# Kernel tuning notes

Measured on AMD Instinct MI355X. Metric: run time of the kernel, lower is better.

The kernel has to match this reference:

```python
import jax, jax.numpy as jnp
import numpy as np

NUM_NODES = 100000
NUM_EDGES = 1600000
FEAT = 128
HID = 128
NUM_GRAPHS = 512


def setup_inputs() -> dict:
    key = jax.random.key(0)
    ks = jax.random.split(key, 8)
    x = jax.random.normal(ks[0], (NUM_NODES, FEAT), dtype=jnp.float32)
    edge_index = jax.random.randint(ks[1], (2, NUM_EDGES), 0, NUM_NODES, dtype=jnp.int64)
    batch = jnp.sort(jax.random.randint(ks[2], (NUM_NODES,), 0, NUM_GRAPHS, dtype=jnp.int64))
    # Glorot-ish init for weights (scale named for clarity)
    s1 = 1.0 / np.sqrt(FEAT)
    s2 = 1.0 / np.sqrt(HID)
    W1 = jax.random.normal(ks[3], (FEAT, HID), dtype=jnp.float32) * s1
    b1 = jnp.zeros((HID,), dtype=jnp.float32)
    W2 = jax.random.normal(ks[4], (HID, HID), dtype=jnp.float32) * s2
    b2 = jnp.zeros((HID,), dtype=jnp.float32)
    Wout = jax.random.normal(ks[5], (HID, 1), dtype=jnp.float32) * s2
    bout = jnp.zeros((1,), dtype=jnp.float32)
    return {"x": x, "edge_index": edge_index, "batch": batch,
            "W1": W1, "b1": b1, "W2": W2, "b2": b2, "Wout": Wout, "bout": bout}


def reference(x, edge_index, batch, W1, b1, W2, b2, Wout, bout):
    N = x.shape[0]
    # PyG GCNConv: add self-loops, symmetric normalization D^-1/2 (A+I) D^-1/2
    loops = jnp.arange(N, dtype=edge_index.dtype)
    src = jnp.concatenate([edge_index[0], loops])  # [E+N]
    dst = jnp.concatenate([edge_index[1], loops])  # [E+N]
    ones = jnp.ones_like(dst, dtype=x.dtype)
    deg = jax.ops.segment_sum(ones, dst, num_segments=N)  # in-degree incl. self-loop
    dinv = jnp.where(deg > 0, jax.lax.rsqrt(deg), 0.0)
    coeff = (dinv[src] * dinv[dst])[:, None]  # [E+N, 1]

    def gcn(h, W, b):
        h = h @ W                                       # [N, H] dense GEMM
        msg = h[src] * coeff                            # gather + scale
        agg = jax.ops.segment_sum(msg, dst, num_segments=N)  # scatter-add
        return agg + b

    h = jax.nn.relu(gcn(x, W1, b1))
    h = jax.nn.relu(gcn(h, W2, b2))

    # global_mean_pool over batch ids
    G = NUM_GRAPHS
    sums = jax.ops.segment_sum(h, batch, num_segments=G)
    cnts = jax.ops.segment_sum(jnp.ones((N,), dtype=h.dtype), batch, num_segments=G)
    pooled = sums / jnp.maximum(cnts, 1.0)[:, None]

    return pooled @ Wout + bout  # [G, 1]
```

## Files before the change

kernel.cpp:

```cpp
#include <hip/hip_runtime.h>
#include <hip/hip_bf16.h>
#include <hip/hip_fp16.h>

#define FEAT 128
#define PSLOTS 64
#define BCAP 5120

typedef _Float16 h8 __attribute__((ext_vector_type(8)));
typedef float f4 __attribute__((ext_vector_type(4)));
typedef float fx2 __attribute__((ext_vector_type(2)));


__global__ __launch_bounds__(256) void k_wt(const float* __restrict__ W1,
                                            const float* __restrict__ W2,
                                            __half* __restrict__ Wt1,
                                            __half* __restrict__ Wt2) {
    int t = blockIdx.x * 256 + threadIdx.x;
    const float* W = (t < 8192) ? W1 : W2;
    __half* Wt     = (t < 8192) ? Wt1 : Wt2;
    int u = t & 8191;
    int n = u >> 6, k2 = (u & 63) * 2;
    float a = W[(size_t)k2 * 128 + n];
    float b = W[(size_t)(k2 + 1) * 128 + n];
    ((__half2*)Wt)[n * 64 + (k2 >> 1)] = __floats2half2_rn(a, b);
}


__device__ __forceinline__ void bin_body(const int* __restrict__ ei, int E, int chunk,
                                         int* __restrict__ cursor,
                                         unsigned* __restrict__ binned, int nb,
                                         int bid, int* smem) {
    int* hist = smem;
    int* base = smem + 512;
    int start = bid * chunk;
    int end = start + chunk; if (end > E) end = E;
    for (int i = threadIdx.x; i < nb; i += 256) hist[i] = 0;
    __syncthreads();
    for (int e = start + threadIdx.x; e < end; e += 256)
        atomicAdd(&hist[ei[E + e] >> 8], 1);
    __syncthreads();
    for (int i = threadIdx.x; i < nb; i += 256) {
        int h = hist[i];
        base[i] = h ? atomicAdd(&cursor[i], h) : 0;
    }
    __syncthreads();
    for (int e = start + threadIdx.x; e < end; e += 256) {
        int s = ei[e];
        int d = ei[E + e];
        int b = d >> 8;
        int pos = atomicAdd(&base[b], 1);
        if (pos < BCAP)
            binned[(size_t)b * BCAP + pos] = (unsigned)s | ((unsigned)(d & 255) << 17);
    }
}


__device__ __forceinline__ void loadA(const __half* p, int quad, h8* a) {
#pragma unroll
    for (int ks = 0; ks < 4; ++ks)
        a[ks] = *(const h8*)(p + ks * 32 + quad * 8);
}
__device__ __forceinline__ void loadA(const float* p, int quad, h8* a) {
#pragma unroll
    for (int ks = 0; ks < 4; ++ks) {
        const float* q = p + ks * 32 + quad * 8;
        float4 f0 = *(const float4*)q;
        float4 f1 = *(const float4*)(q + 4);
        h8 v;
        v[0] = (_Float16)f0.x; v[1] = (_Float16)f0.y;
        v[2] = (_Float16)f0.z; v[3] = (_Float16)f0.w;
        v[4] = (_Float16)f1.x; v[5] = (_Float16)f1.y;
        v[6] = (_Float16)f1.z; v[7] = (_Float16)f1.w;
        a[ks] = v;
    }
}

template <typename TIN>
__device__ __forceinline__ void gemm_body(const TIN* __restrict__ X,
                                          const __half* __restrict__ Wt,
                                          unsigned char* __restrict__ Y, int N,
                                          int bid, _Float16* Bs) {
    {
        const float4* src = (const float4*)Wt;
        float4* dst = (float4*)Bs;
        for (int i = threadIdx.x; i < 2048; i += 256) {
            int n = i >> 4, ch = i & 15;
            dst[n * 16 + (ch ^ (n & 15))] = src[i];
        }
    }
    __syncthreads();

    int lane = threadIdx.x & 63;
    int wave = threadIdx.x >> 6;
    int m = lane & 15;
    int quad = lane >> 4;
    int rowb = bid * 128 + wave * 16;

    h8 a[2][4];
#pragma unroll
    for (int rt = 0; rt < 2; ++rt) {
        int rA = rowb + rt * 64 + m; if (rA >= N) rA = N - 1;
        loadA(X + (size_t)rA * FEAT, quad, a[rt]);
    }

    f4 acc[2][8];
#pragma unroll
    for (int rt = 0; rt < 2; ++rt)
#pragma unroll
        for (int nt = 0; nt < 8; ++nt) acc[rt][nt] = (f4){0.f, 0.f, 0.f, 0.f};

#pragma unroll
    for (int nt = 0; nt < 8; ++nt) {
        const _Float16* bbase = Bs + (nt * 16 + m) * 128;
#pragma unroll
        for (int ks = 0; ks < 4; ++ks) {
            int ch = (ks * 4 + quad) ^ m;
            h8 bfrag = *(const h8*)(bbase + ch * 8);
            acc[0][nt] = __builtin_amdgcn_mfma_f32_16x16x32_f16(a[0][ks], bfrag, acc[0][nt], 0, 0, 0);
            acc[1][nt] = __builtin_amdgcn_mfma_f32_16x16x32_f16(a[1][ks], bfrag, acc[1][nt], 0, 0, 0);
        }
    }

#pragma unroll
    for (int rt = 0; rt < 2; ++rt)
#pragma unroll
    for (int nt = 0; nt < 8; ++nt) {
#pragma unroll
        for (int r = 0; r < 4; ++r) {
            int row = rowb + rt * 64 + quad * 4 + r;
            if (row < N) {
                int pk = __builtin_amdgcn_cvt_pk_fp8_f32(acc[rt][nt][r], acc[rt][nt][r], 0, false);
                Y[(size_t)row * FEAT + nt * 16 + m] = (unsigned char)(pk & 0xFF);
            }
        }
    }
}


__global__ __launch_bounds__(256) void gemm_bin(const float* __restrict__ X,
                                                const __half* __restrict__ Wt1,
                                                unsigned char* __restrict__ Y, int N, int gemm_grid,
                                                const int* __restrict__ ei, int E, int chunk,
                                                int* __restrict__ cursor,
                                                unsigned* __restrict__ binned, int nb) {
    __shared__ __align__(16) char smem[32768];
    if ((int)blockIdx.x < gemm_grid)
        gemm_body<float>(X, Wt1, Y, N, blockIdx.x, (_Float16*)smem);
    else
        bin_body(ei, E, chunk, cursor, binned, nb, blockIdx.x - gemm_grid, (int*)smem);
}


template <typename TIN>
__global__ __launch_bounds__(256) void gemm_mfma(const TIN* __restrict__ X,
                                                 const __half* __restrict__ Wt,
                                                 unsigned char* __restrict__ Y, int N) {
    __shared__ __align__(16) _Float16 Bs[128 * 128];
    gemm_body<TIN>(X, Wt, Y, N, blockIdx.x, Bs);
}


__global__ __launch_bounds__(256) void k_deg_fill(const unsigned* __restrict__ binned,
                                                  const int* __restrict__ cursor,
                                                  int N, int* __restrict__ deg,
                                                  int* __restrict__ rowstart,
                                                  float* __restrict__ dinv,
                                                  int* __restrict__ meta) {
    __shared__ int ld[256];
    __shared__ int sc[256];
    __shared__ int cur[256];
    int b = blockIdx.x;
    int cnt = cursor[b]; if (cnt > BCAP) cnt = BCAP;
    int s = b * BCAP, e = s + cnt;
    ld[threadIdx.x] = 0;
    __syncthreads();
    for (int i = s + threadIdx.x; i < e; i += 256)
        atomicAdd(&ld[binned[i] >> 17], 1);
    __syncthreads();
    int d = ld[threadIdx.x];
    sc[threadIdx.x] = d;
    __syncthreads();
    for (int off = 1; off < 256; off <<= 1) {
        int t = (threadIdx.x >= off) ? sc[threadIdx.x - off] : 0;
        __syncthreads();
        sc[threadIdx.x] += t;
        __syncthreads();
    }
    int rs = s + sc[threadIdx.x] - d;
    cur[threadIdx.x] = rs;
    int v = (b << 8) + threadIdx.x;
    if (v < N) {
        deg[v] = d;
        rowstart[v] = rs;
        dinv[v] = rsqrtf((float)d + 1.0f);
    }
    __syncthreads();
    for (int i = s + threadIdx.x; i < e; i += 256) {
        unsigned p = binned[i];
        int src = (int)(p & 0x1FFFF);
        int drl = (int)(p >> 17);
        int pos = atomicAdd(&cur[drl], 1);
        meta[pos] = src << 7;
    }
}


template <bool POOL>
__global__ __launch_bounds__(256) void agg_relu(const unsigned char* __restrict__ Y,
                                                const float* __restrict__ dinv,
                                                const int* __restrict__ rowstart,
                                                const int* __restrict__ degc,
                                                const int* __restrict__ meta,
                                                const float* __restrict__ bias,
                                                __half* __restrict__ H, int N,
                                                const float* __restrict__ Wout,
                                                const int* __restrict__ batch,
                                                float* __restrict__ gsum, int G) {
    int wid  = (blockIdx.x * 256 + threadIdx.x) >> 6;
    int lane = threadIdx.x & 63;
    if (wid >= N) return;
    int v = wid;
    float dv = dinv[v];

    const char* Yb = (const char*)Y;
    int lb = lane * 2;

    fx2 yv = __builtin_amdgcn_cvt_pk_f32_fp8(
        (int)*(const unsigned short*)(Y + (size_t)v * FEAT + lb), false);
    float selfc = dv * dv;
    float accx = selfc * yv.x;
    float accy = selfc * yv.y;

    int base = rowstart[v];
    int n = degc[v];
    for (int i0 = 0; i0 < n; i0 += 64) {
        int m = n - i0; if (m > 64) m = 64;
        int sl = 0; float cl = 0.f;
        if (lane < m) {
            sl = meta[base + i0 + lane];
            cl = dinv[sl >> 7] * dv;
        }
        for (int i = 0; i < m; i += 8) {
            int   o0 = __shfl(sl, i + 0), o1 = __shfl(sl, i + 1);
            int   o2 = __shfl(sl, i + 2), o3 = __shfl(sl, i + 3);
            int   o4 = __shfl(sl, i + 4), o5 = __shfl(sl, i + 5);
            int   o6 = __shfl(sl, i + 6), o7 = __shfl(sl, i + 7);
            float c0 = __shfl(cl, i + 0), c1 = __shfl(cl, i + 1);
            float c2 = __shfl(cl, i + 2), c3 = __shfl(cl, i + 3);
            float c4 = __shfl(cl, i + 4), c5 = __shfl(cl, i + 5);
            float c6 = __shfl(cl, i + 6), c7 = __shfl(cl, i + 7);
            unsigned short u0 = *(const unsigned short*)(Yb + o0 + lb);
            unsigned short u1 = *(const unsigned short*)(Yb + o1 + lb);
            unsigned short u2 = *(const unsigned short*)(Yb + o2 + lb);
            unsigned short u3 = *(const unsigned short*)(Yb + o3 + lb);
            unsigned short u4 = *(const unsigned short*)(Yb + o4 + lb);
            unsigned short u5 = *(const unsigned short*)(Yb + o5 + lb);
            unsigned short u6 = *(const unsigned short*)(Yb + o6 + lb);
            unsigned short u7 = *(const unsigned short*)(Yb + o7 + lb);
            fx2 y0 = __builtin_amdgcn_cvt_pk_f32_fp8((int)u0, false);
            fx2 y1 = __builtin_amdgcn_cvt_pk_f32_fp8((int)u1, false);
            fx2 y2 = __builtin_amdgcn_cvt_pk_f32_fp8((int)u2, false);
            fx2 y3 = __builtin_amdgcn_cvt_pk_f32_fp8((int)u3, false);
            fx2 y4 = __builtin_amdgcn_cvt_pk_f32_fp8((int)u4, false);
            fx2 y5 = __builtin_amdgcn_cvt_pk_f32_fp8((int)u5, false);
            fx2 y6 = __builtin_amdgcn_cvt_pk_f32_fp8((int)u6, false);
            fx2 y7 = __builtin_amdgcn_cvt_pk_f32_fp8((int)u7, false);
            accx += c0 * y0.x; accy += c0 * y0.y;
            accx += c1 * y1.x; accy += c1 * y1.y;
            accx += c2 * y2.x; accy += c2 * y2.y;
            accx += c3 * y3.x; accy += c3 * y3.y;
            accx += c4 * y4.x; accy += c4 * y4.y;
            accx += c5 * y5.x; accy += c5 * y5.y;
            accx += c6 * y6.x; accy += c6 * y6.y;
            accx += c7 * y7.x; accy += c7 * y7.y;
        }
    }
    float2 b = ((const float2*)bias)[lane];
    float hx = fmaxf(accx + b.x, 0.f);
    float hy = fmaxf(accy + b.y, 0.f);
    if (POOL) {
        float2 wo = ((const float2*)Wout)[lane];
        float s = hx * wo.x + hy * wo.y;
        s += __shfl_xor(s, 1);
        s += __shfl_xor(s, 2);
        s += __shfl_xor(s, 4);
        s += __shfl_xor(s, 8);
        s += __shfl_xor(s, 16);
        s += __shfl_xor(s, 32);
        if (lane == 0) {
            int slot = blockIdx.x & (PSLOTS - 1);
            atomicAdd(&gsum[slot * G + batch[v]], s);
        }
    } else {
        ((__half2*)(H + (size_t)v * FEAT))[lane] = __floats2half2_rn(hx, hy);
    }
}


__global__ __launch_bounds__(256) void k_head(const float* __restrict__ gsum,
                                              const int* __restrict__ batch, int N, int G,
                                              const float* __restrict__ bout,
                                              float* __restrict__ out) {
    int g = blockIdx.x * 256 + threadIdx.x;
    if (g >= G) return;
    float s = 0.f;
#pragma unroll 8
    for (int k = 0; k < PSLOTS; ++k) s += gsum[k * G + g];
    int lo = 0, hi = N;
    while (lo < hi) { int mid = (lo + hi) >> 1; if (batch[mid] < g) lo = mid + 1; else hi = mid; }
    int start = lo;
    lo = start; hi = N;
    while (lo < hi) { int mid = (lo + hi) >> 1; if (batch[mid] < g + 1) lo = mid + 1; else hi = mid; }
    int cnt = lo - start;
    out[g] = s / (float)(cnt > 0 ? cnt : 1) + bout[0];
}


extern "C" void kernel_launch(void* const* d_in, const int* in_sizes, int n_in,
                              void* d_out, int out_size, void* d_ws, size_t ws_size,
                              hipStream_t stream) {
    const float* x    = (const float*)d_in[0];
    const int*   ei   = (const int*)d_in[1];
    const int*   batch= (const int*)d_in[2];
    const float* W1   = (const float*)d_in[3];
    const float* b1   = (const float*)d_in[4];
    const float* W2   = (const float*)d_in[5];
    const float* b2   = (const float*)d_in[6];
    const float* Wout = (const float*)d_in[7];
    const float* bout = (const float*)d_in[8];

    int N = in_sizes[0] / FEAT;
    int E = in_sizes[1] / 2;
    int G = out_size;
    int nb = (N + 255) >> 8;

    char* ws = (char*)d_ws;
    size_t off = 0;
    auto alloc = [&](size_t bytes) -> void* {
        void* p = ws + off;
        off += (bytes + 255) & ~(size_t)255;
        return p;
    };
    unsigned char* bufY = (unsigned char*)alloc((size_t)N * FEAT);
    __half* bufH     = (__half*)alloc((size_t)N * FEAT * 2);
    __half* Wt1      = (__half*)alloc((size_t)FEAT * FEAT * 2);
    __half* Wt2      = (__half*)alloc((size_t)FEAT * FEAT * 2);
    float* dinv      = (float*)alloc((size_t)N * 4);
    int*   deg       = (int*)alloc((size_t)N * 4);
    int*   rowstart  = (int*)alloc((size_t)N * 4);
    float* gsum      = (float*)alloc((size_t)PSLOTS * G * 4 + (size_t)nb * 4);
    int*   cursor    = (int*)(gsum + (size_t)PSLOTS * G);
    unsigned* binned = (unsigned*)alloc((size_t)nb * BCAP * 4);
    int*   meta      = (int*)alloc((size_t)nb * BCAP * 4);

    int gemm_grid = (N + 127) / 128;
    int agg_grid  = (N + 3) / 4;
    int chunk = (E + 255) / 256;

    hipMemsetAsync(gsum, 0, (size_t)PSLOTS * G * 4 + (size_t)nb * 4, stream);
    k_wt<<<64, 256, 0, stream>>>(W1, W2, Wt1, Wt2);
    gemm_bin<<<gemm_grid + 256, 256, 0, stream>>>(x, Wt1, bufY, N, gemm_grid,
                                                  ei, E, chunk, cursor, binned, nb);
    k_deg_fill<<<nb, 256, 0, stream>>>(binned, cursor, N, deg, rowstart, dinv, meta);
    agg_relu<false><<<agg_grid, 256, 0, stream>>>(bufY, dinv, rowstart, deg, meta, b1, bufH, N,
                                                  nullptr, nullptr, nullptr, 0);
    gemm_mfma<__half><<<gemm_grid, 256, 0, stream>>>(bufH, Wt2, bufY, N);
    agg_relu<true><<<agg_grid, 256, 0, stream>>>(bufY, dinv, rowstart, deg, meta, b2, nullptr, N,
                                                 Wout, batch, gsum, G);
    k_head<<<(G + 255) / 256, 256, 0, stream>>>(gsum, batch, N, G, bout, (float*)d_out);
}
```

Before: 288.9 us.

## Fold source dinv into GEMM epilogue and simplify aggregation gather loop

Splits the symmetric normalization so the GEMM epilogue multiplies each row by dinv[src] before the fp8 store, and the aggregation multiplies the final sum once by dinv[dst]. This removes the per-edge dinv gather, the coefficient shuffles and the multiplies from the aggregation inner loop. Tail lanes point at a zeroed padding row, so the gather loop can unroll to 16 without masking. Because the first GEMM now needs dinv, it runs after the degree kernel instead of overlapping with edge binning. The weight transpose is fused into a binning launch with more blocks, and scaling before fp8 quantization changes rounding.

After: 290.7 us. Within noise of the previous version (+0.6%).

```diff
diff --git a/kernel.cpp b/kernel.cpp
--- a/kernel.cpp
+++ b/kernel.cpp
@@ -5,17 +5,18 @@
 #define FEAT 128
 #define PSLOTS 64
 #define BCAP 5120
+#define NBIN 1024
 
 typedef _Float16 h8 __attribute__((ext_vector_type(8)));
 typedef float f4 __attribute__((ext_vector_type(4)));
 typedef float fx2 __attribute__((ext_vector_type(2)));
 
 
-__global__ __launch_bounds__(256) void k_wt(const float* __restrict__ W1,
-                                            const float* __restrict__ W2,
-                                            __half* __restrict__ Wt1,
-                                            __half* __restrict__ Wt2) {
-    int t = blockIdx.x * 256 + threadIdx.x;
+__device__ __forceinline__ void wt_body(const float* __restrict__ W1,
+                                        const float* __restrict__ W2,
+                                        __half* __restrict__ Wt1,
+                                        __half* __restrict__ Wt2, int bid) {
+    int t = bid * 256 + threadIdx.x;
     const float* W = (t < 8192) ? W1 : W2;
     __half* Wt     = (t < 8192) ? Wt1 : Wt2;
     int u = t & 8191;
@@ -24,7 +25,6 @@
     float b = W[(size_t)(k2 + 1) * 128 + n];
     ((__half2*)Wt)[n * 64 + (k2 >> 1)] = __floats2half2_rn(a, b);
 }
-
 
 __device__ __forceinline__ void bin_body(const int* __restrict__ ei, int E, int chunk,
                                          int* __restrict__ cursor,
@@ -52,6 +52,20 @@
         if (pos < BCAP)
             binned[(size_t)b * BCAP + pos] = (unsigned)s | ((unsigned)(d & 255) << 17);
     }
+}
+
+__global__ __launch_bounds__(256) void bin_wt(const int* __restrict__ ei, int E, int chunk,
+                                              int* __restrict__ cursor,
+                                              unsigned* __restrict__ binned, int nb,
+                                              const float* __restrict__ W1,
+                                              const float* __restrict__ W2,
+                                              __half* __restrict__ Wt1,
+                                              __half* __restrict__ Wt2) {
+    __shared__ int smem[1024];
+    if ((int)blockIdx.x < NBIN)
+        bin_body(ei, E, chunk, cursor, binned, nb, blockIdx.x, smem);
+    else
+        wt_body(W1, W2, Wt1, Wt2, blockIdx.x - NBIN);
 }
 
 
@@ -79,6 +93,7 @@
 __device__ __forceinline__ void gemm_body(const TIN* __restrict__ X,
                                           const __half* __restrict__ Wt,
                                           unsigned char* __restrict__ Y, int N,
+                                          const float* __restrict__ scale,
                                           int bid, _Float16* Bs) {
     {
         const float4* src = (const float4*)Wt;
@@ -124,39 +139,27 @@
 #pragma unroll
     for (int rt = 0; rt < 2; ++rt)
 #pragma unroll
-    for (int nt = 0; nt < 8; ++nt) {
-#pragma unroll
-        for (int r = 0; r < 4; ++r) {
-            int row = rowb + rt * 64 + quad * 4 + r;
-            if (row < N) {
-                int pk = __builtin_amdgcn_cvt_pk_fp8_f32(acc[rt][nt][r], acc[rt][nt][r], 0, false);
+    for (int r = 0; r < 4; ++r) {
+        int row = rowb + rt * 64 + quad * 4 + r;
+        if (row < N) {
+            float sc = scale[row];
+#pragma unroll
+            for (int nt = 0; nt < 8; ++nt) {
+                float v = sc * acc[rt][nt][r];
+                int pk = __builtin_amdgcn_cvt_pk_fp8_f32(v, v, 0, false);
                 Y[(size_t)row * FEAT + nt * 16 + m] = (unsigned char)(pk & 0xFF);
             }
         }
     }
 }
-
-
-__global__ __launch_bounds__(256) void gemm_bin(const float* __restrict__ X,
-                                                const __half* __restrict__ Wt1,
-                                                unsigned char* __restrict__ Y, int N, int gemm_grid,
-                                                const int* __restrict__ ei, int E, int chunk,
-                                                int* __restrict__ cursor,
-                                                unsigned* __restrict__ binned, int nb) {
-    __shared__ __align__(16) char smem[32768];
-    if ((int)blockIdx.x < gemm_grid)
-        gemm_body<float>(X, Wt1, Y, N, blockIdx.x, (_Float16*)smem);
-    else
-        bin_body(ei, E, chunk, cursor, binned, nb, blockIdx.x - gemm_grid, (int*)smem);
-}
-
 
 template <typename TIN>
 __global__ __launch_bounds__(256) void gemm_mfma(const TIN* __restrict__ X,
                                                  const __half* __restrict__ Wt,
-                                                 unsigned char* __restrict__ Y, int N) {
+                                                 unsigned char* __restrict__ Y, int N,
+                                                 const float* __restrict__ scale) {
     __shared__ __align__(16) _Float16 Bs[128 * 128];
-    gemm_body<TIN>(X, Wt, Y, N, blockIdx.x, Bs);
+    gemm_body<TIN>(X, Wt, Y, N, scale, blockIdx.x, Bs);
 }
 
 
@@ -221,63 +224,40 @@
     if (wid >= N) return;
     int v = wid;
     float dv = dinv[v];
+    int zoff = N << 7;
 
     const char* Yb = (const char*)Y;
     int lb = lane * 2;
 
     fx2 yv = __builtin_amdgcn_cvt_pk_f32_fp8(
         (int)*(const unsigned short*)(Y + (size_t)v * FEAT + lb), false);
-    float selfc = dv * dv;
-    float accx = selfc * yv.x;
-    float accy = selfc * yv.y;
+    float accx = yv.x;
+    float accy = yv.y;
 
     int base = rowstart[v];
     int n = degc[v];
     for (int i0 = 0; i0 < n; i0 += 64) {
         int m = n - i0; if (m > 64) m = 64;
-        int sl = 0; float cl = 0.f;
-        if (lane < m) {
-            sl = meta[base + i0 + lane];
-            cl = dinv[sl >> 7] * dv;
-        }
-        for (int i = 0; i < m; i += 8) {
-            int   o0 = __shfl(sl, i + 0), o1 = __shfl(sl, i + 1);
-            int   o2 = __shfl(sl, i + 2), o3 = __shfl(sl, i + 3);
-            int   o4 = __shfl(sl, i + 4), o5 = __shfl(sl, i + 5);
-            int   o6 = __shfl(sl, i + 6), o7 = __shfl(sl, i + 7);
-            float c0 = __shfl(cl, i + 0), c1 = __shfl(cl, i + 1);
-            float c2 = __shfl(cl, i + 2), c3 = __shfl(cl, i + 3);
-            float c4 = __shfl(cl, i + 4), c5 = __shfl(cl, i + 5);
-            float c6 = __shfl(cl, i + 6), c7 = __shfl(cl, i + 7);
-            unsigned short u0 = *(const unsigned short*)(Yb + o0 + lb);
-            unsigned short u1 = *(const unsigned short*)(Yb + o1 + lb);
-            unsigned short u2 = *(const unsigned short*)(Yb + o2 + lb);
-            unsigned short u3 = *(const unsigned short*)(Yb + o3 + lb);
-            unsigned short u4 = *(const unsigned short*)(Yb + o4 + lb);
-            unsigned short u5 = *(const unsigned short*)(Yb + o5 + lb);
-            unsigned short u6 = *(const unsigned short*)(Yb + o6 + lb);
-            unsigned short u7 = *(const unsigned short*)(Yb + o7 + lb);
-            fx2 y0 = __builtin_amdgcn_cvt_pk_f32_fp8((int)u0, false);
-            fx2 y1 = __builtin_amdgcn_cvt_pk_f32_fp8((int)u1, false);
-            fx2 y2 = __builtin_amdgcn_cvt_pk_f32_fp8((int)u2, false);
-            fx2 y3 = __builtin_amdgcn_cvt_pk_f32_fp8((int)u3, false);
-            fx2 y4 = __builtin_amdgcn_cvt_pk_f32_fp8((int)u4, false);
-            fx2 y5 = __builtin_amdgcn_cvt_pk_f32_fp8((int)u5, false);
-            fx2 y6 = __builtin_amdgcn_cvt_pk_f32_fp8((int)u6, false);
-            fx2 y7 = __builtin_amdgcn_cvt_pk_f32_fp8((int)u7, false);
-            accx += c0 * y0.x; accy += c0 * y0.y;
-            accx += c1 * y1.x; accy += c1 * y1.y;
-            accx += c2 * y2.x; accy += c2 * y2.y;
-            accx += c3 * y3.x; accy += c3 * y3.y;
-            accx += c4 * y4.x; accy += c4 * y4.y;
-            accx += c5 * y5.x; accy += c5 * y5.y;
-            accx += c6 * y6.x; accy += c6 * y6.y;
-            accx += c7 * y7.x; accy += c7 * y7.y;
+        int sl = (lane < m) ? meta[base + i0 + lane] : zoff;
+        for (int i = 0; i < m; i += 16) {
+            int o[16];
+            unsigned short u[16];
+#pragma unroll
+            for (int j = 0; j < 16; ++j) o[j] = __shfl(sl, i + j);
+#pragma unroll
+            for (int j = 0; j < 16; ++j)
+                u[j] = *(const unsigned short*)(Yb + o[j] + lb);
+#pragma unroll
+            for (int j = 0; j < 16; ++j) {
+                fx2 y = __builtin_amdgcn_cvt_pk_f32_fp8((int)u[j], false);
+                accx += y.x;
+                accy += y.y;
+            }
         }
     }
     float2 b = ((const float2*)bias)[lane];
-    float hx = fmaxf(accx + b.x, 0.f);
-    float hy = fmaxf(accy + b.y, 0.f);
+    float hx = fmaxf(dv * accx + b.x, 0.f);
+    float hy = fmaxf(dv * accy + b.y, 0.f);
     if (POOL) {
         float2 wo = ((const float2*)Wout)[lane];
         float s = hx * wo.x + hy * wo.y;
@@ -341,7 +321,7 @@
         off += (bytes + 255) & ~(size_t)255;
         return p;
     };
-    unsigned char* bufY = (unsigned char*)alloc((size_t)N * FEAT);
+    unsigned char* bufY = (unsigned char*)alloc((size_t)(N + 1) * FEAT);
     __half* bufH     = (__half*)alloc((size_t)N * FEAT * 2);
     __half* Wt1      = (__half*)alloc((size_t)FEAT * FEAT * 2);
     __half* Wt2      = (__half*)alloc((size_t)FEAT * FEAT * 2);
@@ -355,16 +335,17 @@
 
     int gemm_grid = (N + 127) / 128;
     int agg_grid  = (N + 3) / 4;
-    int chunk = (E + 255) / 256;
+    int chunk = (E + NBIN - 1) / NBIN;
 
     hipMemsetAsync(gsum, 0, (size_t)PSLOTS * G * 4 + (size_t)nb * 4, stream);
-    k_wt<<<64, 256, 0, stream>>>(W1, W2, Wt1, Wt2);
-    gemm_bin<<<gemm_grid + 256, 256, 0, stream>>>(x, Wt1, bufY, N, gemm_grid,
-                                                  ei, E, chunk, cursor, binned, nb);
+    hipMemsetAsync(bufY + (size_t)N * FEAT, 0, FEAT, stream);
+    bin_wt<<<NBIN + 64, 256, 0, stream>>>(ei, E, chunk, cursor, binned, nb,
+                                          W1, W2, Wt1, Wt2);
     k_deg_fill<<<nb, 256, 0, stream>>>(binned, cursor, N, deg, rowstart, dinv, meta);
+    gemm_mfma<float><<<gemm_grid, 256, 0, stream>>>(x, Wt1, bufY, N, dinv);
     agg_relu<false><<<agg_grid, 256, 0, stream>>>(bufY, dinv, rowstart, deg, meta, b1, bufH, N,
                                                   nullptr, nullptr, nullptr, 0);
-    gemm_mfma<__half><<<gemm_grid, 256, 0, stream>>>(bufH, Wt2, bufY, N);
+    gemm_mfma<__half><<<gemm_grid, 256, 0, stream>>>(bufH, Wt2, bufY, N, dinv);
     agg_relu<true><<<agg_grid, 256, 0, stream>>>(bufY, dinv, rowstart, deg, meta, b2, nullptr, N,
                                                  Wout, batch, gsum, G);
     k_head<<<(G + 255) / 256, 256, 0, stream>>>(gsum, batch, N, G, bout, (float*)d_out);
```
